# Kernel tuning notes

Hardware: AMD Instinct MI355X
Metric: run time of the kernel (lower is better)

Reference implementation:

```python
import jax, jax.numpy as jnp
import numpy as np

B, N, D, H = 4, 2048, 256, 4
HD = D // H


def _linear(x, W, b):
    return x @ W.T + b


def _rotate_half(x):
    # pairs (x0,x1) -> (-x1, x0)
    x1 = x[..., ::2]
    x2 = x[..., 1::2]
    return jnp.stack((-x2, x1), axis=-1).reshape(x.shape)


def _layernorm(x, g, b, eps=1e-5):
    m = jnp.mean(x, axis=-1, keepdims=True)
    v = jnp.mean((x - m) ** 2, axis=-1, keepdims=True)
    return (x - m) / jnp.sqrt(v + eps) * g + b


def _ffn(x, W1, b1, g, be, W2, b2):
    h = _linear(x, W1, b1)
    h = _layernorm(h, g, be)
    h = jax.nn.gelu(h, approximate=False)
    return _linear(h, W2, b2)


def _self_block(x, enc, Wqkv, bqkv, Wout, bout, W1, b1, g, be, W2, b2):
    Bq, Nq, _ = x.shape
    qkv = _linear(x, Wqkv, bqkv).reshape(Bq, Nq, H, HD, 3).transpose(0, 2, 1, 3, 4)  # [B,H,N,HD,3]
    q, k, v = qkv[..., 0], qkv[..., 1], qkv[..., 2]
    q = q * enc[0] + _rotate_half(q) * enc[1]
    k = k * enc[0] + _rotate_half(k) * enc[1]
    scale = HD ** -0.5
    sim = jnp.einsum('bhid,bhjd->bhij', q, k) * scale
    attn = jax.nn.softmax(sim, axis=-1)
    ctx = jnp.einsum('bhij,bhjd->bhid', attn, v)
    msg = _linear(ctx.transpose(0, 2, 1, 3).reshape(Bq, Nq, D), Wout, bout)
    return x + _ffn(jnp.concatenate([x, msg], axis=-1), W1, b1, g, be, W2, b2)


def _cross_block(x0, x1, Wqk, bqk, Wv, bv, Wo, bo, W1, b1, g, be, W2, b2):
    def heads(t):
        return t.reshape(t.shape[0], t.shape[1], H, HD).transpose(0, 2, 1, 3)  # [B,H,N,HD]
    qk0 = heads(_linear(x0, Wqk, bqk))
    qk1 = heads(_linear(x1, Wqk, bqk))
    v0 = heads(_linear(x0, Wv, bv))
    v1 = heads(_linear(x1, Wv, bv))
    s = (HD ** -0.5) ** 0.5
    qk0 = qk0 * s
    qk1 = qk1 * s
    sim = jnp.einsum('bhid,bhjd->bhij', qk0, qk1)
    attn01 = jax.nn.softmax(sim, axis=-1)   # over j (x1 tokens)
    attn10 = jax.nn.softmax(sim, axis=-2)   # over i (x0 tokens)
    m0 = jnp.einsum('bhij,bhjd->bhid', attn01, v1)
    m1 = jnp.einsum('bhij,bhid->bhjd', attn10, v0)
    def unheads(t):
        return t.transpose(0, 2, 1, 3).reshape(t.shape[0], t.shape[2], D)
    m0 = _linear(unheads(m0), Wo, bo)
    m1 = _linear(unheads(m1), Wo, bo)
    x0 = x0 + _ffn(jnp.concatenate([x0, m0], axis=-1), W1, b1, g, be, W2, b2)
    x1 = x1 + _ffn(jnp.concatenate([x1, m1], axis=-1), W1, b1, g, be, W2, b2)
    return x0, x1


def setup_inputs() -> dict:
    key = jax.random.key(0)
    ks = jax.random.split(key, 32)
    std = 0.05

    def rn(k, shape, s=std):
        return jax.random.normal(k, shape, dtype=jnp.float32) * s

    def enc(k):
        ang = jax.random.uniform(k, (B, 1, N, HD // 2), dtype=jnp.float32) * (2 * np.pi)
        cos = jnp.repeat(jnp.cos(ang), 2, axis=-1)
        sin = jnp.repeat(jnp.sin(ang), 2, axis=-1)
        return jnp.stack([cos, sin], axis=0)  # [2,B,1,N,HD]

    return {
        'desc0': rn(ks[0], (B, N, D), 1.0),
        'desc1': rn(ks[1], (B, N, D), 1.0),
        'enc0': enc(ks[2]),
        'enc1': enc(ks[3]),
        's_Wqkv': rn(ks[4], (3 * D, D)), 's_bqkv': jnp.zeros((3 * D,), jnp.float32),
        's_Wout': rn(ks[5], (D, D)), 's_bout': jnp.zeros((D,), jnp.float32),
        's_W1': rn(ks[6], (2 * D, 2 * D)), 's_b1': jnp.zeros((2 * D,), jnp.float32),
        's_g': jnp.ones((2 * D,), jnp.float32), 's_be': jnp.zeros((2 * D,), jnp.float32),
        's_W2': rn(ks[7], (D, 2 * D)), 's_b2': jnp.zeros((D,), jnp.float32),
        'c_Wqk': rn(ks[8], (D, D)), 'c_bqk': jnp.zeros((D,), jnp.float32),
        'c_Wv': rn(ks[9], (D, D)), 'c_bv': jnp.zeros((D,), jnp.float32),
        'c_Wo': rn(ks[10], (D, D)), 'c_bo': jnp.zeros((D,), jnp.float32),
        'c_W1': rn(ks[11], (2 * D, 2 * D)), 'c_b1': jnp.zeros((2 * D,), jnp.float32),
        'c_g': jnp.ones((2 * D,), jnp.float32), 'c_be': jnp.zeros((2 * D,), jnp.float32),
        'c_W2': rn(ks[12], (D, 2 * D)), 'c_b2': jnp.zeros((D,), jnp.float32),
    }


def reference(desc0, desc1, enc0, enc1,
              s_Wqkv, s_bqkv, s_Wout, s_bout, s_W1, s_b1, s_g, s_be, s_W2, s_b2,
              c_Wqk, c_bqk, c_Wv, c_bv, c_Wo, c_bo, c_W1, c_b1, c_g, c_be, c_W2, c_b2):
    d0 = _self_block(desc0, enc0, s_Wqkv, s_bqkv, s_Wout, s_bout, s_W1, s_b1, s_g, s_be, s_W2, s_b2)
    d1 = _self_block(desc1, enc1, s_Wqkv, s_bqkv, s_Wout, s_bout, s_W1, s_b1, s_g, s_be, s_W2, s_b2)
    return _cross_block(d0, d1, c_Wqk, c_bqk, c_Wv, c_bv, c_Wo, c_bo, c_W1, c_b1, c_g, c_be, c_W2, c_b2)
```

## Files before the change

### kernel.cpp

```cpp
#include <hip/hip_runtime.h>
#include <cstddef>

#define NTOK 2048
#define BDIM 4
#define DIM 256
#define NHEAD 4
#define MROWS 8192
#define M2 16384
#define NMu ((size_t)MROWS * DIM)

typedef unsigned short u16;
typedef __attribute__((ext_vector_type(8))) short short8;
typedef __attribute__((ext_vector_type(4))) float f32x4;

__device__ __forceinline__ u16 f2bf(float x) {
  union { float f; unsigned u; } c; c.f = x;
  unsigned r = c.u + 0x7FFFu + ((c.u >> 16) & 1u);
  return (u16)(r >> 16);
}
__device__ __forceinline__ float bf2f(u16 u) {
  union { unsigned u; float f; } c; c.u = ((unsigned)u) << 16;
  return c.f;
}

__device__ __forceinline__ void glds16(const void* g, void* l) {
  __builtin_amdgcn_global_load_lds(
      (const __attribute__((address_space(1))) unsigned int*)g,
      (__attribute__((address_space(3))) unsigned int*)l, 16, 0, 0);
}

__global__ __launch_bounds__(256) void gemm_bf16_kernel(
    const u16* __restrict__ A, int lda,
    const u16* __restrict__ A2, int lda2, int kSplit,
    const u16* __restrict__ W,
    const float* __restrict__ bias, float oscale,
    const u16* __restrict__ resb, int ldrb,
    float* __restrict__ Yf, int ldyf,
    u16* __restrict__ Yb, int ldyb,
    int K)
{
  __shared__ u16 As[128 * 32];
  __shared__ u16 Bs[128 * 32];
  const int t = threadIdx.x;
  const int m0 = blockIdx.y * 128, n0 = blockIdx.x * 128;
  const int r4 = t >> 2, c8 = (t & 3) * 8;
  const int lane = t & 63, w = t >> 6;
  const int cl = lane & 15, quad = lane >> 4;
  const int wm = (w >> 1) * 64, wn = (w & 1) * 64;

  f32x4 acc[4][4];
#pragma unroll
  for (int i = 0; i < 4; ++i)
#pragma unroll
    for (int j = 0; j < 4; ++j) acc[i][j] = (f32x4){0.f, 0.f, 0.f, 0.f};

  for (int k0 = 0; k0 < K; k0 += 32) {
    const u16* Ab; int la; int kk;
    if (k0 < kSplit) { Ab = A; la = lda; kk = k0; }
    else             { Ab = A2; la = lda2; kk = k0 - kSplit; }
    const u16* ag = Ab + (size_t)(m0 + r4) * la + kk + c8;
    const u16* bg = W + (size_t)(n0 + r4) * K + k0 + c8;
    __syncthreads();
    glds16(ag, &As[t * 8]);
    glds16(ag + (size_t)64 * la, &As[2048 + t * 8]);
    glds16(bg, &Bs[t * 8]);
    glds16(bg + (size_t)64 * K, &Bs[2048 + t * 8]);
    __syncthreads();

    short8 af[4], bfr[4];
#pragma unroll
    for (int i = 0; i < 4; ++i)
      af[i] = *(const short8*)&As[(wm + i * 16 + cl) * 32 + quad * 8];
#pragma unroll
    for (int i = 0; i < 4; ++i)
      bfr[i] = *(const short8*)&Bs[(wn + i * 16 + cl) * 32 + quad * 8];
#pragma unroll
    for (int mt = 0; mt < 4; ++mt)
#pragma unroll
      for (int nt = 0; nt < 4; ++nt)
        acc[mt][nt] = __builtin_amdgcn_mfma_f32_16x16x32_bf16(
            af[mt], bfr[nt], acc[mt][nt], 0, 0, 0);
  }

#pragma unroll
  for (int mt = 0; mt < 4; ++mt)
#pragma unroll
    for (int nt = 0; nt < 4; ++nt) {
      const int colg = n0 + wn + nt * 16 + cl;
      const float bs = bias[colg];
#pragma unroll
      for (int r = 0; r < 4; ++r) {
        const int rowg = m0 + wm + mt * 16 + quad * 4 + r;
        float v = (acc[mt][nt][r] + bs) * oscale;
        if (resb) v += bf2f(resb[(size_t)rowg * ldrb + colg]);
        if (Yf) Yf[(size_t)rowg * ldyf + colg] = v;
        if (Yb) Yb[(size_t)rowg * ldyb + colg] = f2bf(v);
      }
    }
}

__global__ __launch_bounds__(256) void gemm_n64_kernel(
    const u16* __restrict__ A, int lda,
    const u16* __restrict__ A2, int lda2, int kSplit,
    const u16* __restrict__ W,
    const float* __restrict__ bias, float oscale,
    const u16* __restrict__ resb, int ldrb,
    float* __restrict__ Yf, int ldyf,
    u16* __restrict__ Yb, int ldyb,
    int K)
{
  __shared__ u16 As[128 * 32];
  __shared__ u16 Bs[64 * 32];
  const int t = threadIdx.x;
  const int m0 = blockIdx.y * 128, n0 = blockIdx.x * 64;
  const int r4 = t >> 2, c8 = (t & 3) * 8;
  const int lane = t & 63, w = t >> 6;
  const int cl = lane & 15, quad = lane >> 4;
  const int wm = (w >> 1) * 64, wn = (w & 1) * 32;

  f32x4 acc[4][2];
#pragma unroll
  for (int i = 0; i < 4; ++i)
#pragma unroll
    for (int j = 0; j < 2; ++j) acc[i][j] = (f32x4){0.f, 0.f, 0.f, 0.f};

  for (int k0 = 0; k0 < K; k0 += 32) {
    const u16* Ab; int la; int kk;
    if (k0 < kSplit) { Ab = A; la = lda; kk = k0; }
    else             { Ab = A2; la = lda2; kk = k0 - kSplit; }
    const u16* ag = Ab + (size_t)(m0 + r4) * la + kk + c8;
    const u16* bg = W + (size_t)(n0 + r4) * K + k0 + c8;
    __syncthreads();
    glds16(ag, &As[t * 8]);
    glds16(ag + (size_t)64 * la, &As[2048 + t * 8]);
    glds16(bg, &Bs[t * 8]);
    __syncthreads();

    short8 af[4], bfr[2];
#pragma unroll
    for (int i = 0; i < 4; ++i)
      af[i] = *(const short8*)&As[(wm + i * 16 + cl) * 32 + quad * 8];
#pragma unroll
    for (int j = 0; j < 2; ++j)
      bfr[j] = *(const short8*)&Bs[(wn + j * 16 + cl) * 32 + quad * 8];
#pragma unroll
    for (int mt = 0; mt < 4; ++mt)
#pragma unroll
      for (int nt = 0; nt < 2; ++nt)
        acc[mt][nt] = __builtin_amdgcn_mfma_f32_16x16x32_bf16(
            af[mt], bfr[nt], acc[mt][nt], 0, 0, 0);
  }

#pragma unroll
  for (int mt = 0; mt < 4; ++mt)
#pragma unroll
    for (int nt = 0; nt < 2; ++nt) {
      const int colg = n0 + wn + nt * 16 + cl;
      const float bs = bias[colg];
#pragma unroll
      for (int r = 0; r < 4; ++r) {
        const int rowg = m0 + wm + mt * 16 + quad * 4 + r;
        float v = (acc[mt][nt][r] + bs) * oscale;
        if (resb) v += bf2f(resb[(size_t)rowg * ldrb + colg]);
        if (Yf) Yf[(size_t)rowg * ldyf + colg] = v;
        if (Yb) Yb[(size_t)rowg * ldyb + colg] = f2bf(v);
      }
    }
}

__global__ __launch_bounds__(256) void rope_repack_kernel(
    const u16* __restrict__ qkv, const float* __restrict__ enc0,
    const float* __restrict__ enc1,
    u16* __restrict__ Q, u16* __restrict__ K, u16* __restrict__ V)
{
  const int idx = blockIdx.x * blockDim.x + threadIdx.x;
  const int i = idx & 31;
  const int h = (idx >> 5) & 3;
  const int m = idx >> 7;
  const int half = m >> 13;
  const int lm = m & (MROWS - 1);
  const float* enc = half ? enc1 : enc0;
  const u16* src = qkv + (size_t)m * 768 + h * 192 + i * 6;
  const unsigned a0 = *(const unsigned*)(src);
  const unsigned a1 = *(const unsigned*)(src + 2);
  const unsigned a2 = *(const unsigned*)(src + 4);
  const float q0 = bf2f((u16)a0), k0 = bf2f((u16)(a0 >> 16));
  const float v0 = bf2f((u16)a1), q1 = bf2f((u16)(a1 >> 16));
  const float k1 = bf2f((u16)a2), v1 = bf2f((u16)(a2 >> 16));
  const float c = enc[(size_t)lm * 64 + 2 * i];
  const float s = enc[(size_t)MROWS * 64 + (size_t)lm * 64 + 2 * i];
  const size_t o = (size_t)m * 256 + h * 64 + 2 * i;
  *(unsigned*)(Q + o) = (unsigned)f2bf((q0 * c - q1 * s) * 0.125f) |
                        ((unsigned)f2bf((q1 * c + q0 * s) * 0.125f) << 16);
  *(unsigned*)(K + o) = (unsigned)f2bf(k0 * c - k1 * s) |
                        ((unsigned)f2bf(k1 * c + k0 * s) << 16);
  *(unsigned*)(V + o) = (unsigned)f2bf(v0) | ((unsigned)f2bf(v1) << 16);
}

__global__ __launch_bounds__(256) void transpose_v_kernel(
    const u16* __restrict__ in, u16* __restrict__ out)
{
  __shared__ u16 Tl[64][72];
  const int bz = blockIdx.z, h = blockIdx.y;
  const int n0 = blockIdx.x * 64;
  const int t = threadIdx.x;
  {
    const int row = t >> 2, c16 = (t & 3) * 16;
    const u16* src = in + (size_t)(bz * NTOK + n0 + row) * 256 + h * 64 + c16;
    *(uint4*)&Tl[row][c16] = *(const uint4*)src;
    *(uint4*)&Tl[row][c16 + 8] = *(const uint4*)(src + 8);
  }
  __syncthreads();
  const int d = t >> 2, qr = t & 3;
  union { u16 u[16]; uint4 v[2]; } pk;
#pragma unroll
  for (int j = 0; j < 16; ++j) pk.u[j] = Tl[qr * 16 + j][d];
  u16* dst = out + ((size_t)((bz * NHEAD + h) * 64 + d)) * NTOK + n0 + qr * 16;
  *(uint4*)dst = pk.v[0];
  *(uint4*)(dst + 8) = pk.v[1];
}

__global__ __launch_bounds__(256, 4) void attn3_kernel(
    const u16* __restrict__ Qb, const u16* __restrict__ Kb,
    const u16* __restrict__ Vtb,
    u16* __restrict__ Po, float* __restrict__ Pm, float* __restrict__ Pl,
    int cross)
{
  __shared__ u16 Ks[64 * 72];
  __shared__ u16 Vs[64 * 72];
  __shared__ u16 QPs[128 * 72];
  const int y = blockIdx.y, z = blockIdx.z;
  const int h2 = y >> 4, b = (y >> 2) & 3, h = y & 3;
  const int kh = cross ? (1 - h2) : h2;
  const int qrowbase = (h2 * 4 + b) * NTOK;
  const int krowbase = (kh * 4 + b) * NTOK + z * 1024;
  const int vz = kh * 4 + b;
  const int n0 = blockIdx.x * 128;
  const int t = threadIdx.x, lane = t & 63, w = t >> 6;
  const int cl = lane & 15, quad = lane >> 4;

  {
    const int row = t >> 1, c32 = (t & 1) * 32;
    const u16* src = Qb + (size_t)(qrowbase + n0 + row) * 256 + h * 64 + c32;
    uint4 v0 = *(const uint4*)src;
    uint4 v1 = *(const uint4*)(src + 8);
    uint4 v2 = *(const uint4*)(src + 16);
    uint4 v3 = *(const uint4*)(src + 24);
    u16* d = &QPs[row * 72 + c32];
    *(uint4*)d = v0; *(uint4*)(d + 8) = v1;
    *(uint4*)(d + 16) = v2; *(uint4*)(d + 24) = v3;
  }
  __syncthreads();
  const int q0 = w * 32;
  short8 bq[2][2];
#pragma unroll
  for (int c = 0; c < 2; ++c) {
    bq[c][0] = *(const short8*)&QPs[(q0 + c * 16 + cl) * 72 + quad * 8];
    bq[c][1] = *(const short8*)&QPs[(q0 + c * 16 + cl) * 72 + quad * 8 + 32];
  }

  float m_r[2] = {-1e30f, -1e30f}, l_r[2] = {0.f, 0.f};
  f32x4 o[2][4];
#pragma unroll
  for (int c = 0; c < 2; ++c)
#pragma unroll
    for (int i = 0; i < 4; ++i) o[c][i] = (f32x4){0.f, 0.f, 0.f, 0.f};

  const int srow = t >> 2, sc16 = (t & 3) * 16;
  const u16* Kg = Kb + (size_t)(krowbase + srow) * 256 + h * 64 + sc16;
  const u16* Vg = Vtb + ((size_t)(vz * NHEAD + h) * 64 + srow) * NTOK + z * 1024 + sc16;
  uint4 ka0 = *(const uint4*)Kg, ka1 = *(const uint4*)(Kg + 8);
  uint4 va0 = *(const uint4*)Vg, va1 = *(const uint4*)(Vg + 8);

  for (int tile = 0; tile < 16; ++tile) {
    __syncthreads();
    *(uint4*)&Ks[srow * 72 + sc16] = ka0;
    *(uint4*)&Ks[srow * 72 + sc16 + 8] = ka1;
    *(uint4*)&Vs[srow * 72 + sc16] = va0;
    *(uint4*)&Vs[srow * 72 + sc16 + 8] = va1;
    __syncthreads();
    if (tile < 15) {
      Kg += 64 * 256; Vg += 64;
      ka0 = *(const uint4*)Kg; ka1 = *(const uint4*)(Kg + 8);
      va0 = *(const uint4*)Vg; va1 = *(const uint4*)(Vg + 8);
    }

    f32x4 sf[2][4];
#pragma unroll
    for (int kb = 0; kb < 4; ++kb) {
      short8 ak0 = *(const short8*)&Ks[(kb * 16 + cl) * 72 + quad * 8];
      short8 ak1 = *(const short8*)&Ks[(kb * 16 + cl) * 72 + quad * 8 + 32];
#pragma unroll
      for (int c = 0; c < 2; ++c) {
        f32x4 acc = (f32x4){0.f, 0.f, 0.f, 0.f};
        acc = __builtin_amdgcn_mfma_f32_16x16x32_bf16(ak0, bq[c][0], acc, 0, 0, 0);
        acc = __builtin_amdgcn_mfma_f32_16x16x32_bf16(ak1, bq[c][1], acc, 0, 0, 0);
        sf[c][kb] = acc;
      }
    }

#pragma unroll
    for (int c = 0; c < 2; ++c) {
      float mx = sf[c][0][0];
#pragma unroll
      for (int kb = 0; kb < 4; ++kb)
#pragma unroll
        for (int r = 0; r < 4; ++r) mx = fmaxf(mx, sf[c][kb][r]);
      mx = fmaxf(mx, __shfl_xor(mx, 16));
      mx = fmaxf(mx, __shfl_xor(mx, 32));
      const float mn = fmaxf(m_r[c], mx);
      const float alpha = __expf(m_r[c] - mn);
      m_r[c] = mn;
      float rs = 0.f;
#pragma unroll
      for (int kb = 0; kb < 4; ++kb)
#pragma unroll
        for (int r = 0; r < 4; ++r) {
          const float p = __expf(sf[c][kb][r] - mn);
          sf[c][kb][r] = p; rs += p;
        }
      rs += __shfl_xor(rs, 16);
      rs += __shfl_xor(rs, 32);
      l_r[c] = l_r[c] * alpha + rs;
#pragma unroll
      for (int db = 0; db < 4; ++db) o[c][db] *= alpha;
#pragma unroll
      for (int kb = 0; kb < 4; ++kb) {
        unsigned d0 = __builtin_amdgcn_perm(__float_as_uint(sf[c][kb][1]),
                                            __float_as_uint(sf[c][kb][0]), 0x07060302u);
        unsigned d1 = __builtin_amdgcn_perm(__float_as_uint(sf[c][kb][3]),
                                            __float_as_uint(sf[c][kb][2]), 0x07060302u);
        uint2 pk; pk.x = d0; pk.y = d1;
        *(uint2*)&QPs[(q0 + c * 16 + cl) * 72 + kb * 16 + quad * 4] = pk;
      }
    }

    short8 bp[2][2];
#pragma unroll
    for (int c = 0; c < 2; ++c) {
      bp[c][0] = *(const short8*)&QPs[(q0 + c * 16 + cl) * 72 + quad * 8];
      bp[c][1] = *(const short8*)&QPs[(q0 + c * 16 + cl) * 72 + quad * 8 + 32];
    }
#pragma unroll
    for (int db = 0; db < 4; ++db) {
      short8 av0 = *(const short8*)&Vs[(db * 16 + cl) * 72 + quad * 8];
      short8 av1 = *(const short8*)&Vs[(db * 16 + cl) * 72 + quad * 8 + 32];
#pragma unroll
      for (int c = 0; c < 2; ++c) {
        o[c][db] = __builtin_amdgcn_mfma_f32_16x16x32_bf16(av0, bp[c][0], o[c][db], 0, 0, 0);
        o[c][db] = __builtin_amdgcn_mfma_f32_16x16x32_bf16(av1, bp[c][1], o[c][db], 0, 0, 0);
      }
    }
  }

#pragma unroll
  for (int c = 0; c < 2; ++c) {
    const int rp = z * 65536 + y * 2048 + n0 + q0 + c * 16 + cl;
#pragma unroll
    for (int db = 0; db < 4; ++db) {
      ushort4 st;
      st.x = f2bf(o[c][db][0]); st.y = f2bf(o[c][db][1]);
      st.z = f2bf(o[c][db][2]); st.w = f2bf(o[c][db][3]);
      *(ushort4*)(Po + (size_t)rp * 64 + db * 16 + quad * 4) = st;
    }
    if (quad == 0) { Pm[rp] = m_r[c]; Pl[rp] = l_r[c]; }
  }
}

__global__ __launch_bounds__(256) void attn_combine_kernel(
    const u16* __restrict__ Po, const float* __restrict__ Pm,
    const float* __restrict__ Pl, u16* __restrict__ Ou)
{
  const int rowi = blockIdx.x * 4 + (threadIdx.x >> 6);
  const int lane = threadIdx.x & 63;
  const float m0 = Pm[rowi], m1 = Pm[65536 + rowi];
  const float l0 = Pl[rowi], l1 = Pl[65536 + rowi];
  const float M = fmaxf(m0, m1);
  const float e0 = __expf(m0 - M), e1 = __expf(m1 - M);
  const float inv = 1.f / (e0 * l0 + e1 * l1);
  const float o0 = bf2f(Po[(size_t)rowi * 64 + lane]);
  const float o1 = bf2f(Po[(size_t)65536 * 64 + (size_t)rowi * 64 + lane]);
  const float val = (e0 * o0 + e1 * o1) * inv;
  const int y = rowi >> 11, q = rowi & 2047;
  const int bz = y >> 2, h = y & 3;
  Ou[(size_t)(bz * NTOK + q) * 256 + h * 64 + lane] = f2bf(val);
}

__global__ __launch_bounds__(256) void ln_gelu_kernel(
    const u16* __restrict__ Hm, const float* __restrict__ g,
    const float* __restrict__ be, u16* __restrict__ out)
{
  const int rowi = blockIdx.x * 4 + (threadIdx.x >> 6);
  const int lane = threadIdx.x & 63;
  const u16* row = Hm + (size_t)rowi * 512 + lane * 8;
  u16* orow = out + (size_t)rowi * 512 + lane * 8;
  uint4 raw = *(const uint4*)row;
  float x[8];
  const unsigned* rw = (const unsigned*)&raw;
#pragma unroll
  for (int i = 0; i < 4; ++i) {
    x[2 * i]     = bf2f((u16)rw[i]);
    x[2 * i + 1] = bf2f((u16)(rw[i] >> 16));
  }
  float s = 0.f;
#pragma unroll
  for (int i = 0; i < 8; ++i) s += x[i];
#pragma unroll
  for (int off = 32; off; off >>= 1) s += __shfl_xor(s, off);
  const float mean = s * (1.f / 512.f);
  float s2 = 0.f;
#pragma unroll
  for (int i = 0; i < 8; ++i) { const float d = x[i] - mean; s2 += d * d; }
#pragma unroll
  for (int off = 32; off; off >>= 1) s2 += __shfl_xor(s2, off);
  const float rstd = rsqrtf(s2 * (1.f / 512.f) + 1e-5f);
  unsigned ov[4];
#pragma unroll
  for (int i = 0; i < 4; ++i) {
    const int c = lane * 8 + 2 * i;
    const float y0 = (x[2 * i] - mean) * rstd * g[c] + be[c];
    const float y1 = (x[2 * i + 1] - mean) * rstd * g[c + 1] + be[c + 1];
    const float g0 = 0.5f * y0 * (1.f + erff(y0 * 0.70710678118654752f));
    const float g1 = 0.5f * y1 * (1.f + erff(y1 * 0.70710678118654752f));
    ov[i] = (unsigned)f2bf(g0) | ((unsigned)f2bf(g1) << 16);
  }
  *(uint4*)orow = *(uint4*)ov;
}

__global__ __launch_bounds__(256) void pack_desc_kernel(
    const float* __restrict__ in0, const float* __restrict__ in1,
    u16* __restrict__ out)
{
  const float* in = blockIdx.y ? in1 : in0;
  const size_t i4 = ((size_t)blockIdx.x * 256 + threadIdx.x) * 4;
  float4 v = *(const float4*)(in + i4);
  ushort4 o;
  o.x = f2bf(v.x); o.y = f2bf(v.y); o.z = f2bf(v.z); o.w = f2bf(v.w);
  *(ushort4*)(out + blockIdx.y * NMu + i4) = o;
}

__global__ __launch_bounds__(256) void pack_weights_kernel(
    const float* w0, const float* w1, const float* w2, const float* w3,
    const float* w4, const float* w5, const float* w6, const float* w7,
    const float* w8, u16* __restrict__ out)
{
  const int idx4 = (blockIdx.x * 256 + threadIdx.x) * 4;
  const float* src; int off;
  if      (idx4 <  196608) { src = w0; off = idx4; }
  else if (idx4 <  262144) { src = w1; off = idx4 - 196608; }
  else if (idx4 <  524288) { src = w2; off = idx4 - 262144; }
  else if (idx4 <  655360) { src = w3; off = idx4 - 524288; }
  else if (idx4 <  720896) { src = w4; off = idx4 - 655360; }
  else if (idx4 <  786432) { src = w5; off = idx4 - 720896; }
  else if (idx4 <  851968) { src = w6; off = idx4 - 786432; }
  else if (idx4 < 1114112) { src = w7; off = idx4 - 851968; }
  else                     { src = w8; off = idx4 - 1114112; }
  float4 v = *(const float4*)(src + off);
  ushort4 o;
  o.x = f2bf(v.x); o.y = f2bf(v.y); o.z = f2bf(v.z); o.w = f2bf(v.w);
  *(ushort4*)(out + idx4) = o;
}

static inline void launch_gemm(const u16* A, int lda, const u16* A2, int lda2,
                               int kSplit, const u16* W, const float* bias,
                               float oscale, const u16* resb, int ldrb,
                               float* Yf, int ldyf, u16* Yb, int ldyb,
                               int N, int K, hipStream_t s)
{
  if (N == 256) {
    dim3 g(N / 64, M2 / 128);
    hipLaunchKernelGGL(gemm_n64_kernel, g, dim3(256), 0, s,
                       A, lda, A2, lda2, kSplit, W, bias, oscale,
                       resb, ldrb, Yf, ldyf, Yb, ldyb, K);
  } else {
    dim3 g(N / 128, M2 / 128);
    hipLaunchKernelGGL(gemm_bf16_kernel, g, dim3(256), 0, s,
                       A, lda, A2, lda2, kSplit, W, bias, oscale,
                       resb, ldrb, Yf, ldyf, Yb, ldyb, K);
  }
}

extern "C" void kernel_launch(void* const* d_in, const int* in_sizes, int n_in,
                              void* d_out, int out_size, void* d_ws, size_t ws_size,
                              hipStream_t stream) {
  const float* desc0  = (const float*)d_in[0];
  const float* desc1  = (const float*)d_in[1];
  const float* enc0   = (const float*)d_in[2];
  const float* enc1   = (const float*)d_in[3];
  const float* s_Wqkv = (const float*)d_in[4];
  const float* s_bqkv = (const float*)d_in[5];
  const float* s_Wout = (const float*)d_in[6];
  const float* s_bout = (const float*)d_in[7];
  const float* s_W1   = (const float*)d_in[8];
  const float* s_b1   = (const float*)d_in[9];
  const float* s_g    = (const float*)d_in[10];
  const float* s_be   = (const float*)d_in[11];
  const float* s_W2   = (const float*)d_in[12];
  const float* s_b2   = (const float*)d_in[13];
  const float* c_Wqk  = (const float*)d_in[14];
  const float* c_bqk  = (const float*)d_in[15];
  const float* c_Wv   = (const float*)d_in[16];
  const float* c_bv   = (const float*)d_in[17];
  const float* c_Wo   = (const float*)d_in[18];
  const float* c_bo   = (const float*)d_in[19];
  const float* c_W1   = (const float*)d_in[20];
  const float* c_b1   = (const float*)d_in[21];
  const float* c_g    = (const float*)d_in[22];
  const float* c_be   = (const float*)d_in[23];
  const float* c_W2   = (const float*)d_in[24];
  const float* c_b2   = (const float*)d_in[25];

  u16* U = (u16*)d_ws;
  u16* descb = U + 0 * NMu;
  u16* qkvb  = U + 2 * NMu;
  u16* ctxb  = U + 2 * NMu;
  u16* msgb  = U + 4 * NMu;
  u16* Qu    = U + 8 * NMu;
  u16* Ku    = U + 10 * NMu;
  u16* Vu    = U + 12 * NMu;
  u16* Vt    = U + 14 * NMu;
  u16* hb2   = U + 12 * NMu;
  u16* Po    = U + 16 * NMu;
  u16* hbufb = U + 16 * NMu;
  float* Pm  = (float*)(U + 20 * NMu);
  float* Pl  = Pm + 2 * 65536;
  u16* s_b   = U + 21 * NMu;
  u16* wb    = U + 23 * NMu;

  u16* Wqkvb = wb;
  u16* Woutb = wb + 196608;
  u16* W1b   = wb + 262144;
  u16* W2b   = wb + 524288;
  u16* cWqkb = wb + 655360;
  u16* cWvb  = wb + 720896;
  u16* cWob  = wb + 786432;
  u16* cW1b  = wb + 851968;
  u16* cW2b  = wb + 1114112;

  float* outf = (float*)d_out;

  const dim3 attn_grid(NTOK / 128, 32, 2);
  const dim3 tv_grid(NTOK / 64, NHEAD, 8);
  const int rope_blocks = (M2 * 128) / 256;
  const int lng_blocks  = M2 / 4;
  const int comb_blocks = 65536 / 4;
  const dim3 desc_grid((unsigned)(NMu / 4 / 256), 2);
  const float cscale = 0.35355339059327373f;

  hipLaunchKernelGGL(pack_weights_kernel, dim3(1216), dim3(256), 0, stream,
                     s_Wqkv, s_Wout, s_W1, s_W2, c_Wqk, c_Wv, c_Wo, c_W1, c_W2, wb);
  hipLaunchKernelGGL(pack_desc_kernel, desc_grid, dim3(256), 0, stream,
                     desc0, desc1, descb);

  launch_gemm(descb, 256, nullptr, 0, 1 << 30, Wqkvb, s_bqkv, 1.f,
              nullptr, 0, nullptr, 0, qkvb, 768, 768, 256, stream);
  hipLaunchKernelGGL(rope_repack_kernel, dim3(rope_blocks), dim3(256), 0, stream,
                     qkvb, enc0, enc1, Qu, Ku, Vu);
  hipLaunchKernelGGL(transpose_v_kernel, tv_grid, dim3(256), 0, stream, Vu, Vt);
  hipLaunchKernelGGL(attn3_kernel, attn_grid, dim3(256), 0, stream,
                     Qu, Ku, Vt, Po, Pm, Pl, 0);
  hipLaunchKernelGGL(attn_combine_kernel, dim3(comb_blocks), dim3(256), 0, stream,
                     Po, Pm, Pl, ctxb);
  launch_gemm(ctxb, 256, nullptr, 0, 1 << 30, Woutb, s_bout, 1.f,
              nullptr, 0, nullptr, 0, msgb, 256, 256, 256, stream);
  launch_gemm(descb, 256, msgb, 256, 256, W1b, s_b1, 1.f,
              nullptr, 0, nullptr, 0, hbufb, 512, 512, 512, stream);
  hipLaunchKernelGGL(ln_gelu_kernel, dim3(lng_blocks), dim3(256), 0, stream,
                     hbufb, s_g, s_be, hb2);
  launch_gemm(hb2, 512, nullptr, 0, 1 << 30, W2b, s_b2, 1.f,
              descb, 256, nullptr, 0, s_b, 256, 256, 512, stream);

  u16* qkb = Qu;
  u16* vb  = Ku;
  launch_gemm(s_b, 256, nullptr, 0, 1 << 30, cWqkb, c_bqk, cscale,
              nullptr, 0, nullptr, 0, qkb, 256, 256, 256, stream);
  launch_gemm(s_b, 256, nullptr, 0, 1 << 30, cWvb, c_bv, 1.f,
              nullptr, 0, nullptr, 0, vb, 256, 256, 256, stream);
  hipLaunchKernelGGL(transpose_v_kernel, tv_grid, dim3(256), 0, stream, vb, Vt);
  hipLaunchKernelGGL(attn3_kernel, attn_grid, dim3(256), 0, stream,
                     qkb, qkb, Vt, Po, Pm, Pl, 1);
  hipLaunchKernelGGL(attn_combine_kernel, dim3(comb_blocks), dim3(256), 0, stream,
                     Po, Pm, Pl, ctxb);
  launch_gemm(ctxb, 256, nullptr, 0, 1 << 30, cWob, c_bo, 1.f,
              nullptr, 0, nullptr, 0, msgb, 256, 256, 256, stream);
  launch_gemm(s_b, 256, msgb, 256, 256, cW1b, c_b1, 1.f,
              nullptr, 0, nullptr, 0, hbufb, 512, 512, 512, stream);
  hipLaunchKernelGGL(ln_gelu_kernel, dim3(lng_blocks), dim3(256), 0, stream,
                     hbufb, c_g, c_be, hb2);
  launch_gemm(hb2, 512, nullptr, 0, 1 << 30, cW2b, c_b2, 1.f,
              s_b, 256, outf, 256, nullptr, 0, 256, 512, stream);
}
```

Before: 449.8 us.

## Fold output projection into FFN W1, merge cross QK/V GEMM, use exp2 softmax

```diff
diff --git a/kernel.cpp b/kernel.cpp
--- a/kernel.cpp
+++ b/kernel.cpp
@@ -33,10 +33,10 @@
     const u16* __restrict__ A, int lda,
     const u16* __restrict__ A2, int lda2, int kSplit,
     const u16* __restrict__ W,
-    const float* __restrict__ bias, float oscale,
-    const u16* __restrict__ resb, int ldrb,
-    float* __restrict__ Yf, int ldyf,
-    u16* __restrict__ Yb, int ldyb,
+    const float* __restrict__ bias0, const float* __restrict__ bias1,
+    int nsplit, float os0, float os1,
+    u16* __restrict__ Yb0, int ldy0,
+    u16* __restrict__ Yb1, int ldy1,
     int K)
 {
   __shared__ u16 As[128 * 32];
@@ -87,11 +87,77 @@
 #pragma unroll
     for (int nt = 0; nt < 4; ++nt) {
       const int colg = n0 + wn + nt * 16 + cl;
-      const float bs = bias[colg];
+      const bool first = colg < nsplit;
+      const int c2 = first ? colg : colg - nsplit;
+      const float bs = first ? bias0[c2] : bias1[c2];
+      const float os = first ? os0 : os1;
+      u16* yb = first ? Yb0 : Yb1;
+      const int ly = first ? ldy0 : ldy1;
 #pragma unroll
       for (int r = 0; r < 4; ++r) {
         const int rowg = m0 + wm + mt * 16 + quad * 4 + r;
-        float v = (acc[mt][nt][r] + bs) * oscale;
+        yb[(size_t)rowg * ly + c2] = f2bf((acc[mt][nt][r] + bs) * os);
+      }
+    }
+}
+
+__global__ __launch_bounds__(256) void gemm64_kernel(
+    const u16* __restrict__ A, int lda,
+    const u16* __restrict__ W,
+    const float* __restrict__ bias,
+    const u16* __restrict__ resb, int ldrb,
+    float* __restrict__ Yf, int ldyf,
+    u16* __restrict__ Yb, int ldyb,
+    int K)
+{
+  __shared__ u16 As[64 * 32];
+  __shared__ u16 Bs[64 * 32];
+  const int t = threadIdx.x;
+  const int m0 = blockIdx.y * 64, n0 = blockIdx.x * 64;
+  const int r8 = t >> 2, c8 = (t & 3) * 8;
+  const int lane = t & 63, w = t >> 6;
+  const int cl = lane & 15, quad = lane >> 4;
+  const int wm = (w >> 1) * 32, wn = (w & 1) * 32;
+
+  f32x4 acc[2][2];
+#pragma unroll
+  for (int i = 0; i < 2; ++i)
+#pragma unroll
+    for (int j = 0; j < 2; ++j) acc[i][j] = (f32x4){0.f, 0.f, 0.f, 0.f};
+
+  for (int k0 = 0; k0 < K; k0 += 32) {
+    const u16* ag = A + (size_t)(m0 + r8) * lda + k0 + c8;
+    const u16* bg = W + (size_t)(n0 + r8) * K + k0 + c8;
+    __syncthreads();
+    glds16(ag, &As[t * 8]);
+    glds16(bg, &Bs[t * 8]);
+    __syncthreads();
+
+    short8 af[2], bfr[2];
+#pragma unroll
+    for (int i = 0; i < 2; ++i)
+      af[i] = *(const short8*)&As[(wm + i * 16 + cl) * 32 + quad * 8];
+#pragma unroll
+    for (int j = 0; j < 2; ++j)
+      bfr[j] = *(const short8*)&Bs[(wn + j * 16 + cl) * 32 + quad * 8];
+#pragma unroll
+    for (int mt = 0; mt < 2; ++mt)
+#pragma unroll
+      for (int nt = 0; nt < 2; ++nt)
+        acc[mt][nt] = __builtin_amdgcn_mfma_f32_16x16x32_bf16(
+            af[mt], bfr[nt], acc[mt][nt], 0, 0, 0);
+  }
+
+#pragma unroll
+  for (int mt = 0; mt < 2; ++mt)
+#pragma unroll
+    for (int nt = 0; nt < 2; ++nt) {
+      const int colg = n0 + wn + nt * 16 + cl;
+      const float bs = bias[colg];
+#pragma unroll
+      for (int r = 0; r < 4; ++r) {
+        const int rowg = m0 + wm + mt * 16 + quad * 4 + r;
+        float v = acc[mt][nt][r] + bs;
         if (resb) v += bf2f(resb[(size_t)rowg * ldrb + colg]);
         if (Yf) Yf[(size_t)rowg * ldyf + colg] = v;
         if (Yb) Yb[(size_t)rowg * ldyb + colg] = f2bf(v);
@@ -99,73 +165,33 @@
     }
 }
 
-__global__ __launch_bounds__(256) void gemm_n64_kernel(
-    const u16* __restrict__ A, int lda,
-    const u16* __restrict__ A2, int lda2, int kSplit,
-    const u16* __restrict__ W,
-    const float* __restrict__ bias, float oscale,
-    const u16* __restrict__ resb, int ldrb,
-    float* __restrict__ Yf, int ldyf,
-    u16* __restrict__ Yb, int ldyb,
-    int K)
-{
-  __shared__ u16 As[128 * 32];
-  __shared__ u16 Bs[64 * 32];
+__global__ __launch_bounds__(256) void wfuse_kernel(
+    const float* __restrict__ W1, const float* __restrict__ Wo,
+    const float* __restrict__ b1, const float* __restrict__ bo,
+    const float* __restrict__ cW1, const float* __restrict__ cWo,
+    const float* __restrict__ cb1, const float* __restrict__ cbo,
+    u16* __restrict__ W1f, u16* __restrict__ cW1f,
+    float* __restrict__ b1f, float* __restrict__ cb1f)
+{
+  const int n = blockIdx.x, sel = blockIdx.y;
+  const float* Ws = sel ? cW1 : W1;
+  const float* Wos = sel ? cWo : Wo;
+  u16* out = sel ? cW1f : W1f;
+  __shared__ float rowh[256];
   const int t = threadIdx.x;
-  const int m0 = blockIdx.y * 128, n0 = blockIdx.x * 64;
-  const int r4 = t >> 2, c8 = (t & 3) * 8;
-  const int lane = t & 63, w = t >> 6;
-  const int cl = lane & 15, quad = lane >> 4;
-  const int wm = (w >> 1) * 64, wn = (w & 1) * 32;
-
-  f32x4 acc[4][2];
-#pragma unroll
-  for (int i = 0; i < 4; ++i)
-#pragma unroll
-    for (int j = 0; j < 2; ++j) acc[i][j] = (f32x4){0.f, 0.f, 0.f, 0.f};
-
-  for (int k0 = 0; k0 < K; k0 += 32) {
-    const u16* Ab; int la; int kk;
-    if (k0 < kSplit) { Ab = A; la = lda; kk = k0; }
-    else             { Ab = A2; la = lda2; kk = k0 - kSplit; }
-    const u16* ag = Ab + (size_t)(m0 + r4) * la + kk + c8;
-    const u16* bg = W + (size_t)(n0 + r4) * K + k0 + c8;
-    __syncthreads();
-    glds16(ag, &As[t * 8]);
-    glds16(ag + (size_t)64 * la, &As[2048 + t * 8]);
-    glds16(bg, &Bs[t * 8]);
-    __syncthreads();
-
-    short8 af[4], bfr[2];
-#pragma unroll
-    for (int i = 0; i < 4; ++i)
-      af[i] = *(const short8*)&As[(wm + i * 16 + cl) * 32 + quad * 8];
-#pragma unroll
-    for (int j = 0; j < 2; ++j)
-      bfr[j] = *(const short8*)&Bs[(wn + j * 16 + cl) * 32 + quad * 8];
-#pragma unroll
-    for (int mt = 0; mt < 4; ++mt)
-#pragma unroll
-      for (int nt = 0; nt < 2; ++nt)
-        acc[mt][nt] = __builtin_amdgcn_mfma_f32_16x16x32_bf16(
-            af[mt], bfr[nt], acc[mt][nt], 0, 0, 0);
-  }
-
-#pragma unroll
-  for (int mt = 0; mt < 4; ++mt)
-#pragma unroll
-    for (int nt = 0; nt < 2; ++nt) {
-      const int colg = n0 + wn + nt * 16 + cl;
-      const float bs = bias[colg];
-#pragma unroll
-      for (int r = 0; r < 4; ++r) {
-        const int rowg = m0 + wm + mt * 16 + quad * 4 + r;
-        float v = (acc[mt][nt][r] + bs) * oscale;
-        if (resb) v += bf2f(resb[(size_t)rowg * ldrb + colg]);
-        if (Yf) Yf[(size_t)rowg * ldyf + colg] = v;
-        if (Yb) Yb[(size_t)rowg * ldyb + colg] = f2bf(v);
-      }
-    }
+  rowh[t] = Ws[(size_t)n * 512 + 256 + t];
+  out[(size_t)n * 512 + t] = f2bf(Ws[(size_t)n * 512 + t]);
+  __syncthreads();
+  float acc = 0.f;
+  for (int m = 0; m < 256; ++m) acc += rowh[m] * Wos[(size_t)m * 256 + t];
+  out[(size_t)n * 512 + 256 + t] = f2bf(acc);
+  if (t == 0) {
+    const float* bos = sel ? cbo : bo;
+    const float* b1s = sel ? cb1 : b1;
+    float a = b1s[n];
+    for (int m = 0; m < 256; ++m) a += rowh[m] * bos[m];
+    (sel ? cb1f : b1f)[n] = a;
+  }
 }
 
 __global__ __launch_bounds__(256) void rope_repack_kernel(
@@ -189,9 +215,10 @@
   const float k1 = bf2f((u16)a2), v1 = bf2f((u16)(a2 >> 16));
   const float c = enc[(size_t)lm * 64 + 2 * i];
   const float s = enc[(size_t)MROWS * 64 + (size_t)lm * 64 + 2 * i];
+  const float QSC = 0.18033688011112042f;
   const size_t o = (size_t)m * 256 + h * 64 + 2 * i;
-  *(unsigned*)(Q + o) = (unsigned)f2bf((q0 * c - q1 * s) * 0.125f) |
-                        ((unsigned)f2bf((q1 * c + q0 * s) * 0.125f) << 16);
+  *(unsigned*)(Q + o) = (unsigned)f2bf((q0 * c - q1 * s) * QSC) |
+                        ((unsigned)f2bf((q1 * c + q0 * s) * QSC) << 16);
   *(unsigned*)(K + o) = (unsigned)f2bf(k0 * c - k1 * s) |
                         ((unsigned)f2bf(k1 * c + k0 * s) << 16);
   *(unsigned*)(V + o) = (unsigned)f2bf(v0) | ((unsigned)f2bf(v1) << 16);
@@ -309,14 +336,14 @@
       mx = fmaxf(mx, __shfl_xor(mx, 16));
       mx = fmaxf(mx, __shfl_xor(mx, 32));
       const float mn = fmaxf(m_r[c], mx);
-      const float alpha = __expf(m_r[c] - mn);
+      const float alpha = exp2f(m_r[c] - mn);
       m_r[c] = mn;
       float rs = 0.f;
 #pragma unroll
       for (int kb = 0; kb < 4; ++kb)
 #pragma unroll
         for (int r = 0; r < 4; ++r) {
-          const float p = __expf(sf[c][kb][r] - mn);
+          const float p = exp2f(sf[c][kb][r] - mn);
           sf[c][kb][r] = p; rs += p;
         }
       rs += __shfl_xor(rs, 16);
@@ -376,7 +403,7 @@
   const float m0 = Pm[rowi], m1 = Pm[65536 + rowi];
   const float l0 = Pl[rowi], l1 = Pl[65536 + rowi];
   const float M = fmaxf(m0, m1);
-  const float e0 = __expf(m0 - M), e1 = __expf(m1 - M);
+  const float e0 = exp2f(m0 - M), e1 = exp2f(m1 - M);
   const float inv = 1.f / (e0 * l0 + e1 * l1);
   const float o0 = bf2f(Po[(size_t)rowi * 64 + lane]);
   const float o1 = bf2f(Po[(size_t)65536 * 64 + (size_t)rowi * 64 + lane]);
@@ -427,57 +454,30 @@
   *(uint4*)orow = *(uint4*)ov;
 }
 
-__global__ __launch_bounds__(256) void pack_desc_kernel(
-    const float* __restrict__ in0, const float* __restrict__ in1,
-    u16* __restrict__ out)
-{
-  const float* in = blockIdx.y ? in1 : in0;
-  const size_t i4 = ((size_t)blockIdx.x * 256 + threadIdx.x) * 4;
-  float4 v = *(const float4*)(in + i4);
-  ushort4 o;
-  o.x = f2bf(v.x); o.y = f2bf(v.y); o.z = f2bf(v.z); o.w = f2bf(v.w);
-  *(ushort4*)(out + blockIdx.y * NMu + i4) = o;
-}
-
-__global__ __launch_bounds__(256) void pack_weights_kernel(
+__global__ __launch_bounds__(256) void pack_all_kernel(
     const float* w0, const float* w1, const float* w2, const float* w3,
-    const float* w4, const float* w5, const float* w6, const float* w7,
-    const float* w8, u16* __restrict__ out)
-{
-  const int idx4 = (blockIdx.x * 256 + threadIdx.x) * 4;
-  const float* src; int off;
-  if      (idx4 <  196608) { src = w0; off = idx4; }
-  else if (idx4 <  262144) { src = w1; off = idx4 - 196608; }
-  else if (idx4 <  524288) { src = w2; off = idx4 - 262144; }
-  else if (idx4 <  655360) { src = w3; off = idx4 - 524288; }
-  else if (idx4 <  720896) { src = w4; off = idx4 - 655360; }
-  else if (idx4 <  786432) { src = w5; off = idx4 - 720896; }
-  else if (idx4 <  851968) { src = w6; off = idx4 - 786432; }
-  else if (idx4 < 1114112) { src = w7; off = idx4 - 851968; }
-  else                     { src = w8; off = idx4 - 1114112; }
+    const float* w4, const float* d0, const float* d1,
+    u16* __restrict__ wb, u16* __restrict__ descb)
+{
+  const size_t idx4 = ((size_t)blockIdx.x * 256 + threadIdx.x) * 4;
+  const float* src; u16* dst; size_t off;
+  if (idx4 < 589824) {
+    off = idx4; dst = wb + idx4;
+    if      (idx4 < 196608) { src = w0; }
+    else if (idx4 < 327680) { src = w1; off -= 196608; }
+    else if (idx4 < 393216) { src = w2; off -= 327680; }
+    else if (idx4 < 458752) { src = w3; off -= 393216; }
+    else                    { src = w4; off -= 458752; }
+  } else {
+    size_t o = idx4 - 589824;
+    dst = descb + o;
+    if (o < NMu) { src = d0; off = o; }
+    else         { src = d1; off = o - NMu; }
+  }
   float4 v = *(const float4*)(src + off);
-  ushort4 o;
-  o.x = f2bf(v.x); o.y = f2bf(v.y); o.z = f2bf(v.z); o.w = f2bf(v.w);
-  *(ushort4*)(out + idx4) = o;
-}
-
-static inline void launch_gemm(const u16* A, int lda, const u16* A2, int lda2,
-                               int kSplit, const u16* W, const float* bias,
-                               float oscale, const u16* resb, int ldrb,
-                               float* Yf, int ldyf, u16* Yb, int ldyb,
-                               int N, int K, hipStream_t s)
-{
-  if (N == 256) {
-    dim3 g(N / 64, M2 / 128);
-    hipLaunchKernelGGL(gemm_n64_kernel, g, dim3(256), 0, s,
-                       A, lda, A2, lda2, kSplit, W, bias, oscale,
-                       resb, ldrb, Yf, ldyf, Yb, ldyb, K);
-  } else {
-    dim3 g(N / 128, M2 / 128);
-    hipLaunchKernelGGL(gemm_bf16_kernel, g, dim3(256), 0, s,
-                       A, lda, A2, lda2, kSplit, W, bias, oscale,
-                       resb, ldrb, Yf, ldyf, Yb, ldyb, K);
-  }
+  ushort4 ov;
+  ov.x = f2bf(v.x); ov.y = f2bf(v.y); ov.z = f2bf(v.z); ov.w = f2bf(v.w);
+  *(ushort4*)dst = ov;
 }
 
 extern "C" void kernel_launch(void* const* d_in, const int* in_sizes, int n_in,
@@ -514,28 +514,26 @@
   u16* descb = U + 0 * NMu;
   u16* qkvb  = U + 2 * NMu;
   u16* ctxb  = U + 2 * NMu;
-  u16* msgb  = U + 4 * NMu;
   u16* Qu    = U + 8 * NMu;
   u16* Ku    = U + 10 * NMu;
   u16* Vu    = U + 12 * NMu;
   u16* Vt    = U + 14 * NMu;
-  u16* hb2   = U + 12 * NMu;
+  u16* hbufb = U + 12 * NMu;
   u16* Po    = U + 16 * NMu;
-  u16* hbufb = U + 16 * NMu;
+  u16* hb2   = U + 16 * NMu;
   float* Pm  = (float*)(U + 20 * NMu);
   float* Pl  = Pm + 2 * 65536;
+  float* b1f = Pl + 2 * 65536;
+  float* cb1f = b1f + 512;
   u16* s_b   = U + 21 * NMu;
   u16* wb    = U + 23 * NMu;
 
   u16* Wqkvb = wb;
-  u16* Woutb = wb + 196608;
-  u16* W1b   = wb + 262144;
-  u16* W2b   = wb + 524288;
-  u16* cWqkb = wb + 655360;
-  u16* cWvb  = wb + 720896;
-  u16* cWob  = wb + 786432;
-  u16* cW1b  = wb + 851968;
-  u16* cW2b  = wb + 1114112;
+  u16* W2b   = wb + 196608;
+  u16* cQKVb = wb + 327680;
+  u16* cW2b  = wb + 458752;
+  u16* W1f   = wb + 589824;
+  u16* cW1f  = wb + 851968;
 
   float* outf = (float*)d_out;
 
@@ -544,16 +542,20 @@
   const int rope_blocks = (M2 * 128) / 256;
   const int lng_blocks  = M2 / 4;
   const int comb_blocks = 65536 / 4;
-  const dim3 desc_grid((unsigned)(NMu / 4 / 256), 2);
-  const float cscale = 0.35355339059327373f;
-
-  hipLaunchKernelGGL(pack_weights_kernel, dim3(1216), dim3(256), 0, stream,
-                     s_Wqkv, s_Wout, s_W1, s_W2, c_Wqk, c_Wv, c_Wo, c_W1, c_W2, wb);
-  hipLaunchKernelGGL(pack_desc_kernel, desc_grid, dim3(256), 0, stream,
-                     desc0, desc1, descb);
-
-  launch_gemm(descb, 256, nullptr, 0, 1 << 30, Wqkvb, s_bqkv, 1.f,
-              nullptr, 0, nullptr, 0, qkvb, 768, 768, 256, stream);
+  const float BIG = 2.1e9f;
+  (void)BIG;
+  const float csc = 0.42466090014400953f;
+
+  hipLaunchKernelGGL(pack_all_kernel, dim3(4672), dim3(256), 0, stream,
+                     s_Wqkv, s_W2, c_Wqk, c_Wv, c_W2, desc0, desc1, wb, descb);
+  hipLaunchKernelGGL(wfuse_kernel, dim3(512, 2), dim3(256), 0, stream,
+                     s_W1, s_Wout, s_b1, s_bout, c_W1, c_Wo, c_b1, c_bo,
+                     W1f, cW1f, b1f, cb1f);
+
+  hipLaunchKernelGGL(gemm_bf16_kernel, dim3(6, 128), dim3(256), 0, stream,
+                     descb, 256, (const u16*)nullptr, 0, 1 << 30, Wqkvb,
+                     s_bqkv, (const float*)nullptr, 1 << 30, 1.f, 1.f,
+                     qkvb, 768, (u16*)nullptr, 0, 256);
   hipLaunchKernelGGL(rope_repack_kernel, dim3(rope_blocks), dim3(256), 0, stream,
                      qkvb, enc0, enc1, Qu, Ku, Vu);
   hipLaunchKernelGGL(transpose_v_kernel, tv_grid, dim3(256), 0, stream, Vu, Vt);
@@ -561,32 +563,34 @@
                      Qu, Ku, Vt, Po, Pm, Pl, 0);
   hipLaunchKernelGGL(attn_combine_kernel, dim3(comb_blocks), dim3(256), 0, stream,
                      Po, Pm, Pl, ctxb);
-  launch_gemm(ctxb, 256, nullptr, 0, 1 << 30, Woutb, s_bout, 1.f,
-              nullptr, 0, nullptr, 0, msgb, 256, 256, 256, stream);
-  launch_gemm(descb, 256, msgb, 256, 256, W1b, s_b1, 1.f,
-              nullptr, 0, nullptr, 0, hbufb, 512, 512, 512, stream);
+  hipLaunchKernelGGL(gemm_bf16_kernel, dim3(4, 128), dim3(256), 0, stream,
+                     descb, 256, ctxb, 256, 256, W1f,
+                     b1f, (const float*)nullptr, 1 << 30, 1.f, 1.f,
+                     hbufb, 512, (u16*)nullptr, 0, 512);
   hipLaunchKernelGGL(ln_gelu_kernel, dim3(lng_blocks), dim3(256), 0, stream,
                      hbufb, s_g, s_be, hb2);
-  launch_gemm(hb2, 512, nullptr, 0, 1 << 30, W2b, s_b2, 1.f,
-              descb, 256, nullptr, 0, s_b, 256, 256, 512, stream);
+  hipLaunchKernelGGL(gemm64_kernel, dim3(4, 256), dim3(256), 0, stream,
+                     hb2, 512, W2b, s_b2, descb, 256,
+                     (float*)nullptr, 0, s_b, 256, 512);
 
   u16* qkb = Qu;
   u16* vb  = Ku;
-  launch_gemm(s_b, 256, nullptr, 0, 1 << 30, cWqkb, c_bqk, cscale,
-              nullptr, 0, nullptr, 0, qkb, 256, 256, 256, stream);
-  launch_gemm(s_b, 256, nullptr, 0, 1 << 30, cWvb, c_bv, 1.f,
-              nullptr, 0, nullptr, 0, vb, 256, 256, 256, stream);
+  hipLaunchKernelGGL(gemm_bf16_kernel, dim3(4, 128), dim3(256), 0, stream,
+                     s_b, 256, (const u16*)nullptr, 0, 1 << 30, cQKVb,
+                     c_bqk, c_bv, 256, csc, 1.f,
+                     qkb, 256, vb, 256, 256);
   hipLaunchKernelGGL(transpose_v_kernel, tv_grid, dim3(256), 0, stream, vb, Vt);
   hipLaunchKernelGGL(attn3_kernel, attn_grid, dim3(256), 0, stream,
                      qkb, qkb, Vt, Po, Pm, Pl, 1);
   hipLaunchKernelGGL(attn_combine_kernel, dim3(comb_blocks), dim3(256), 0, stream,
                      Po, Pm, Pl, ctxb);
-  launch_gemm(ctxb, 256, nullptr, 0, 1 << 30, cWob, c_bo, 1.f,
-              nullptr, 0, nullptr, 0, msgb, 256, 256, 256, stream);
-  launch_gemm(s_b, 256, msgb, 256, 256, cW1b, c_b1, 1.f,
-              nullptr, 0, nullptr, 0, hbufb, 512, 512, 512, stream);
+  hipLaunchKernelGGL(gemm_bf16_kernel, dim3(4, 128), dim3(256), 0, stream,
+                     s_b, 256, ctxb, 256, 256, cW1f,
+                     cb1f, (const float*)nullptr, 1 << 30, 1.f, 1.f,
+                     hbufb, 512, (u16*)nullptr, 0, 512);
   hipLaunchKernelGGL(ln_gelu_kernel, dim3(lng_blocks), dim3(256), 0, stream,
                      hbufb, c_g, c_be, hb2);
-  launch_gemm(hb2, 512, nullptr, 0, 1 << 30, cW2b, c_b2, 1.f,
-              s_b, 256, outf, 256, nullptr, 0, 256, 512, stream);
-}
+  hipLaunchKernelGGL(gemm64_kernel, dim3(4, 256), dim3(256), 0, stream,
+                     hb2, 512, cW2b, c_b2, s_b, 256,
+                     outf, 256, (u16*)nullptr, 0, 512);
+}
```

Measured after the change: 442.0 us. About the same (-1.7%).
